# Optimization experiments

Hardware: AMD Instinct MI355X
Metric: run time of the kernel (lower is better)

The kernel has to match this reference:

```python
import jax, jax.numpy as jnp
import numpy as np

N, E = 10000, 320000
IN, HID, HEADS, OUT = 1280, 128, 4, 500
NEG_SLOPE = 0.2
BN_EPS = 1e-5


def gat_layer(x, src, dst, W, a_src, a_dst, b, concat):
    """PyG-style GATConv (single weight matrix, additive attention, scatter-softmax)."""
    n = x.shape[0]
    H, C = a_src.shape
    xp = (x @ W).reshape(n, H, C)                      # [N,H,C]
    s = jnp.sum(xp * a_src, axis=-1)                   # [N,H] src attention logits
    d = jnp.sum(xp * a_dst, axis=-1)                   # [N,H] dst attention logits
    e = jax.nn.leaky_relu(s[src] + d[dst], NEG_SLOPE)  # [Etot,H]
    # scatter-softmax over edges sharing the same destination node
    m = jax.ops.segment_max(e, dst, num_segments=n)
    ex = jnp.exp(e - m[dst])
    z = jax.ops.segment_sum(ex, dst, num_segments=n)
    alpha = ex / z[dst]                                # [Etot,H]
    out = jax.ops.segment_sum(alpha[:, :, None] * xp[src], dst, num_segments=n)  # [N,H,C]
    out = out.reshape(n, H * C) if concat else out.mean(axis=1)
    return out + b


def batch_norm(x, gamma, beta):
    mu = x.mean(axis=0)
    var = x.var(axis=0)  # biased, matches torch BN training normalization
    return (x - mu) * jax.lax.rsqrt(var + BN_EPS) * gamma + beta


def setup_inputs() -> dict:
    key = jax.random.key(0)
    ks = jax.random.split(key, 20)
    rn = lambda k, shape, s=0.05: jax.random.normal(k, shape, jnp.float32) * s
    HC = HID * HEADS
    return {
        "x": jax.random.normal(ks[0], (N, IN), jnp.float32),
        "edge_index": jax.random.randint(ks[1], (2, E), 0, N, jnp.int64 if jax.config.jax_enable_x64 else jnp.int32),
        "W1": rn(ks[2], (IN, HC)), "a_src1": rn(ks[3], (HEADS, HID)), "a_dst1": rn(ks[4], (HEADS, HID)), "b1": jnp.zeros((HC,), jnp.float32),
        "g1": jnp.ones((HC,), jnp.float32), "be1": jnp.zeros((HC,), jnp.float32),
        "W2": rn(ks[5], (HC, HC)), "a_src2": rn(ks[6], (HEADS, HID)), "a_dst2": rn(ks[7], (HEADS, HID)), "b2": jnp.zeros((HC,), jnp.float32),
        "g2": jnp.ones((HC,), jnp.float32), "be2": jnp.zeros((HC,), jnp.float32),
        "W3": rn(ks[8], (HC, OUT)), "a_src3": rn(ks[9], (1, OUT)), "a_dst3": rn(ks[10], (1, OUT)), "b3": jnp.zeros((OUT,), jnp.float32),
    }


def reference(x, edge_index, W1, a_src1, a_dst1, b1, g1, be1,
              W2, a_src2, a_dst2, b2, g2, be2, W3, a_src3, a_dst3, b3):
    n = x.shape[0]
    loops = jnp.arange(n, dtype=edge_index.dtype)
    src = jnp.concatenate([edge_index[0], loops])  # PyG add_self_loops=True
    dst = jnp.concatenate([edge_index[1], loops])
    h = gat_layer(x, src, dst, W1, a_src1, a_dst1, b1, concat=True)
    h = jax.nn.elu(batch_norm(h, g1, be1))
    h = gat_layer(h, src, dst, W2, a_src2, a_dst2, b2, concat=True)
    h = jax.nn.elu(batch_norm(h, g2, be2))
    return gat_layer(h, src, dst, W3, a_src3, a_dst3, b3, concat=False)
```

## Files before the change

kernel.cpp:

```cpp
#include <hip/hip_runtime.h>
#include <hip/hip_bf16.h>

#define NNODES 10000
#define NEDGES 320000
#define INF_   1280
#define HID_   128
#define HEADS_ 4
#define OUTF_  500
#define HC_    512
#define NEG_SLOPE 0.2f
#define BN_EPS 1e-5f

typedef __attribute__((ext_vector_type(8))) short short8x;
typedef __attribute__((ext_vector_type(4))) float f32x4;
typedef unsigned short ushort_t;
typedef unsigned int uint_t;

__device__ __forceinline__ ushort_t f2bf(float f) {
    uint_t u = __float_as_uint(f);
    u = (u + 0x7fffu + ((u >> 16) & 1u)) >> 16;
    return (ushort_t)u;
}
__device__ __forceinline__ float bf_lo(uint_t p) { return __uint_as_float(p << 16); }
__device__ __forceinline__ float bf_hi(uint_t p) { return __uint_as_float(p & 0xffff0000u); }
__device__ __forceinline__ float lrelu(float x) { return (x >= 0.f) ? x : NEG_SLOPE * x; }
__device__ __forceinline__ uint_t pack_bf16_rn(float a, float b) {
    __hip_bfloat162 h = __float22bfloat162_rn(make_float2(a, b));
    return *(uint_t*)&h;
}

__global__ void zero_kernel(float* __restrict__ p, size_t n) {
    size_t i = (size_t)blockIdx.x * blockDim.x + threadIdx.x;
    size_t stride = (size_t)gridDim.x * blockDim.x;
    for (; i < n; i += stride) p[i] = 0.0f;
}

#define CVX (NNODES * INF_ / 4)
#define CN1 (HC_ * INF_)
#define CN2 (HC_ * HC_)
#define CN3 (HC_ * HC_)
__global__ void convall_kernel(const float* __restrict__ x,
                               const float* __restrict__ W1,
                               const float* __restrict__ W2,
                               const float* __restrict__ W3,
                               ushort_t* __restrict__ x_bf,
                               ushort_t* __restrict__ Wt1,
                               ushort_t* __restrict__ Wt2,
                               ushort_t* __restrict__ Wt3) {
    int i = blockIdx.x * blockDim.x + threadIdx.x;
    if (i < CVX) {
        float4 v = ((const float4*)x)[i];
        ((uint2*)x_bf)[i] = make_uint2(pack_bf16_rn(v.x, v.y), pack_bf16_rn(v.z, v.w));
    } else if (i < CVX + CN1) {
        int j = i - CVX;
        int n = j / INF_, k = j - n * INF_;
        Wt1[j] = f2bf(W1[(size_t)k * HC_ + n]);
    } else if (i < CVX + CN1 + CN2) {
        int j = i - CVX - CN1;
        int n = j / HC_, k = j - n * HC_;
        Wt2[j] = f2bf(W2[(size_t)k * HC_ + n]);
    } else if (i < CVX + CN1 + CN2 + CN3) {
        int j = i - CVX - CN1 - CN2;
        int n = j / HC_, k = j - n * HC_;
        Wt3[j] = (n < OUTF_) ? f2bf(W3[(size_t)k * OUTF_ + n]) : (ushort_t)0;
    }
}

__global__ void count_kernel(const int* __restrict__ dst, int* __restrict__ counts, int E) {
    int e = blockIdx.x * blockDim.x + threadIdx.x;
    if (e < E) atomicAdd(&counts[dst[e]], 1);
}

__global__ __launch_bounds__(256) void scan1_kernel(const int* __restrict__ counts,
                                                    int* __restrict__ offsets,
                                                    int* __restrict__ bsum, int n) {
    __shared__ int tmp[256];
    int b = blockIdx.x, t = threadIdx.x;
    int i = b * 256 + t;
    int v = (i < n) ? counts[i] : 0;
    tmp[t] = v;
    __syncthreads();
    for (int off = 1; off < 256; off <<= 1) {
        int u = (t >= off) ? tmp[t - off] : 0;
        __syncthreads();
        tmp[t] += u;
        __syncthreads();
    }
    if (i < n) offsets[i] = tmp[t] - v;
    if (t == 255) bsum[b] = tmp[t];
}

__global__ __launch_bounds__(256) void scan3b_kernel(int* __restrict__ offsets,
                                                     int* __restrict__ cursor,
                                                     const int* __restrict__ bsum,
                                                     int nb, int n) {
    __shared__ int base_sh, tot_sh;
    int b = blockIdx.x, t = threadIdx.x;
    if (t == 0) {
        int acc = 0, tot = 0;
        for (int k = 0; k < nb; ++k) { if (k < b) acc += bsum[k]; tot += bsum[k]; }
        base_sh = acc; tot_sh = tot;
    }
    __syncthreads();
    int i = b * 256 + t;
    if (i < n) {
        int v = offsets[i] + base_sh;
        offsets[i] = v;
        cursor[i] = v;
    }
    if (b == nb - 1 && t == 0) offsets[n] = tot_sh;
}

__global__ void scatter_kernel(const int* __restrict__ src, const int* __restrict__ dst,
                               int* __restrict__ cursor, int* __restrict__ esrc, int E) {
    int e = blockIdx.x * blockDim.x + threadIdx.x;
    if (e < E) {
        int p = atomicAdd(&cursor[dst[e]], 1);
        esrc[p] = src[e];
    }
}

#define LDT 40

__global__ __launch_bounds__(256) void gemm_kernel(
    const ushort_t* __restrict__ A,
    const ushort_t* __restrict__ Bt,
    ushort_t* __restrict__ Cb,
    int M, int K)
{
    __shared__ __align__(16) ushort_t As[64 * LDT];
    __shared__ __align__(16) ushort_t Bs[128 * LDT];

    int m0 = blockIdx.y * 64;
    int n0 = blockIdx.x * 128;

    int tid  = threadIdx.x;
    int lane = tid & 63;
    int w    = tid >> 6;
    int wm   = (w & 1) * 32;
    int wn   = (w >> 1) * 64;
    int quad = lane >> 4;
    int c16  = lane & 15;

    f32x4 acc[2][4];
#pragma unroll
    for (int i = 0; i < 2; ++i)
#pragma unroll
        for (int j = 0; j < 4; ++j)
#pragma unroll
            for (int r = 0; r < 4; ++r) acc[i][j][r] = 0.0f;

    int sr = tid >> 2;
    int sk = (tid & 3) * 8;
    int gm = m0 + sr;  if (gm > M - 1) gm = M - 1;
    const ushort_t* aptr = A + (size_t)gm * K + sk;
    int br0 = tid >> 2;
    int bk0 = (tid & 3) * 8;
    int br1 = (256 + tid) >> 2;
    int bk1 = bk0;
    const ushort_t* bptr0 = Bt + (size_t)(n0 + br0) * K + bk0;
    const ushort_t* bptr1 = Bt + (size_t)(n0 + br1) * K + bk1;

    uint4 av  = *(const uint4*)(aptr);
    uint4 bv0 = *(const uint4*)(bptr0);
    uint4 bv1 = *(const uint4*)(bptr1);

    for (int k0 = 0; k0 < K; k0 += 32) {
        *(uint4*)&As[sr * LDT + sk]   = av;
        *(uint4*)&Bs[br0 * LDT + bk0] = bv0;
        *(uint4*)&Bs[br1 * LDT + bk1] = bv1;
        __syncthreads();

        short8x af0 = *(const short8x*)&As[(wm +      c16) * LDT + quad * 8];
        short8x af1 = *(const short8x*)&As[(wm + 16 + c16) * LDT + quad * 8];
        short8x bf[4];
#pragma unroll
        for (int nt = 0; nt < 4; ++nt)
            bf[nt] = *(const short8x*)&Bs[(wn + nt * 16 + c16) * LDT + quad * 8];

        if (k0 + 32 < K) {
            av  = *(const uint4*)(aptr  + k0 + 32);
            bv0 = *(const uint4*)(bptr0 + k0 + 32);
            bv1 = *(const uint4*)(bptr1 + k0 + 32);
        }

#pragma unroll
        for (int nt = 0; nt < 4; ++nt) {
            acc[0][nt] = __builtin_amdgcn_mfma_f32_16x16x32_bf16(af0, bf[nt], acc[0][nt], 0, 0, 0);
            acc[1][nt] = __builtin_amdgcn_mfma_f32_16x16x32_bf16(af1, bf[nt], acc[1][nt], 0, 0, 0);
        }
        __syncthreads();
    }

#pragma unroll
    for (int mt = 0; mt < 2; ++mt) {
#pragma unroll
        for (int r = 0; r < 4; ++r) {
            int row = m0 + wm + mt * 16 + quad * 4 + r;
            if (row < M) {
#pragma unroll
                for (int nt = 0; nt < 4; ++nt) {
                    int col = n0 + wn + nt * 16 + c16;
                    Cb[(size_t)row * 512 + col] = f2bf(acc[mt][nt][r]);
                }
            }
        }
    }
}

template<int H>
__global__ __launch_bounds__(256) void logits_kernel(
    const uint4* __restrict__ xpb4,
    const float* __restrict__ aS, const float* __restrict__ aD,
    float* __restrict__ s_log, float* __restrict__ d_log, int OUTC)
{
    int node = blockIdx.x * 4 + (threadIdx.x >> 6);
    if (node >= NNODES) return;
    int lane = threadIdx.x & 63;
    uint4 p = xpb4[(size_t)node * 64 + lane];
    float xv[8] = {bf_lo(p.x), bf_hi(p.x), bf_lo(p.y), bf_hi(p.y),
                   bf_lo(p.z), bf_hi(p.z), bf_lo(p.w), bf_hi(p.w)};
    int cbase = lane * 8;
    float sv = 0.f, dv = 0.f;
    if (cbase + 7 < OUTC) {
        float4 a0 = ((const float4*)aS)[lane * 2];
        float4 a1 = ((const float4*)aS)[lane * 2 + 1];
        float4 b0 = ((const float4*)aD)[lane * 2];
        float4 b1 = ((const float4*)aD)[lane * 2 + 1];
        sv = xv[0]*a0.x + xv[1]*a0.y + xv[2]*a0.z + xv[3]*a0.w
           + xv[4]*a1.x + xv[5]*a1.y + xv[6]*a1.z + xv[7]*a1.w;
        dv = xv[0]*b0.x + xv[1]*b0.y + xv[2]*b0.z + xv[3]*b0.w
           + xv[4]*b1.x + xv[5]*b1.y + xv[6]*b1.z + xv[7]*b1.w;
    } else {
#pragma unroll
        for (int k = 0; k < 8; ++k) {
            int c = cbase + k;
            if (c < OUTC) { sv += xv[k] * aS[c]; dv += xv[k] * aD[c]; }
        }
    }
    int grp = (H == 4) ? 16 : 64;
    for (int off = 1; off < grp; off <<= 1) {
        sv += __shfl_xor(sv, off);
        dv += __shfl_xor(dv, off);
    }
    if ((lane & (grp - 1)) == 0) {
        int h = (H == 4) ? (lane >> 4) : 0;
        s_log[node * H + h] = sv;
        d_log[node * H + h] = dv;
    }
}

__device__ __forceinline__ void acc8(float* acc, uint4 q, float w) {
    acc[0] += w * bf_lo(q.x); acc[1] += w * bf_hi(q.x);
    acc[2] += w * bf_lo(q.y); acc[3] += w * bf_hi(q.y);
    acc[4] += w * bf_lo(q.z); acc[5] += w * bf_hi(q.z);
    acc[6] += w * bf_lo(q.w); acc[7] += w * bf_hi(q.w);
}

template<int H>
__global__ __launch_bounds__(256) void gather_fused_kernel(
    const uint4* __restrict__ xpb4,
    const int* __restrict__ offsets, const int* __restrict__ esrc,
    const float* __restrict__ s_log,
    const float* __restrict__ d_log,
    const float* __restrict__ bias,
    float* __restrict__ out,
    int OUTC, int ldo)
{
    int id = blockIdx.x;
    int xcd = id & 7;
    int slice = xcd >> 1;
    int sub2 = xcd & 1;
    int wv = threadIdx.x >> 6;
    int node = (id >> 3) * 8 + sub2 * 4 + wv;
    if (node >= NNODES) return;
    int lane = threadIdx.x & 63;
    int esub = lane >> 4;
    int l16 = lane & 15;
    int h = (H == 4) ? slice : 0;
    int rowoff = slice * 16 + l16;

    float dh = d_log[node * H + h];
    float c0 = lrelu(s_log[node * H + h] + dh);

    float acc[8];
    float z;
    if (esub == 0) {
        uint4 p = xpb4[(size_t)node * 64 + rowoff];
        acc[0] = bf_lo(p.x); acc[1] = bf_hi(p.x);
        acc[2] = bf_lo(p.y); acc[3] = bf_hi(p.y);
        acc[4] = bf_lo(p.z); acc[5] = bf_hi(p.z);
        acc[6] = bf_lo(p.w); acc[7] = bf_hi(p.w);
        z = 1.0f;
    } else {
#pragma unroll
        for (int k = 0; k < 8; ++k) acc[k] = 0.f;
        z = 0.f;
    }

    int e0 = offsets[node], e1 = offsets[node + 1];
    int j = e0 + esub;
    for (; j + 12 < e1; j += 16) {
        int s0 = esrc[j], s1 = esrc[j + 4], s2 = esrc[j + 8], s3 = esrc[j + 12];
        uint4 q0 = xpb4[(size_t)s0 * 64 + rowoff];
        uint4 q1 = xpb4[(size_t)s1 * 64 + rowoff];
        uint4 q2 = xpb4[(size_t)s2 * 64 + rowoff];
        uint4 q3 = xpb4[(size_t)s3 * 64 + rowoff];
        float w0 = __expf(lrelu(s_log[s0 * H + h] + dh) - c0);
        float w1 = __expf(lrelu(s_log[s1 * H + h] + dh) - c0);
        float w2 = __expf(lrelu(s_log[s2 * H + h] + dh) - c0);
        float w3 = __expf(lrelu(s_log[s3 * H + h] + dh) - c0);
        acc8(acc, q0, w0);
        acc8(acc, q1, w1);
        acc8(acc, q2, w2);
        acc8(acc, q3, w3);
        z += w0 + w1 + w2 + w3;
    }
    for (; j < e1; j += 4) {
        int s0 = esrc[j];
        uint4 q0 = xpb4[(size_t)s0 * 64 + rowoff];
        float w0 = __expf(lrelu(s_log[s0 * H + h] + dh) - c0);
        acc8(acc, q0, w0);
        z += w0;
    }

#pragma unroll
    for (int k = 0; k < 8; ++k) {
        acc[k] += __shfl_xor(acc[k], 16);
        acc[k] += __shfl_xor(acc[k], 32);
    }
    z += __shfl_xor(z, 16);
    z += __shfl_xor(z, 32);

    if (esub == 0) {
        float zi = 1.0f / z;
        int cbase = slice * 128 + l16 * 8;
        size_t ob = (size_t)node * ldo + cbase;
        if (cbase + 7 < OUTC) {
            float4 o0 = make_float4(acc[0] * zi + bias[cbase + 0], acc[1] * zi + bias[cbase + 1],
                                    acc[2] * zi + bias[cbase + 2], acc[3] * zi + bias[cbase + 3]);
            float4 o1 = make_float4(acc[4] * zi + bias[cbase + 4], acc[5] * zi + bias[cbase + 5],
                                    acc[6] * zi + bias[cbase + 6], acc[7] * zi + bias[cbase + 7]);
            *(float4*)(out + ob) = o0;
            *(float4*)(out + ob + 4) = o1;
        } else {
#pragma unroll
            for (int k = 0; k < 8; ++k) {
                int c = cbase + k;
                if (c < OUTC) out[ob + k] = acc[k] * zi + bias[c];
            }
        }
    }
}

__global__ __launch_bounds__(512) void bn_stats_kernel(const float* __restrict__ h,
                                                       float* __restrict__ psum,
                                                       float* __restrict__ psumsq) {
    int c = threadIdx.x;
    int b = blockIdx.x;
    float sm = 0.f, sq = 0.f;
    for (int r = b; r < NNODES; r += 64) {
        float v = h[(size_t)r * 512 + c];
        sm += v;
        sq += v * v;
    }
    psum[b * 512 + c] = sm;
    psumsq[b * 512 + c] = sq;
}

__global__ __launch_bounds__(512) void bn_finalize_kernel(const float* __restrict__ psum,
                                                          const float* __restrict__ psumsq,
                                                          const float* __restrict__ gamma,
                                                          const float* __restrict__ beta,
                                                          float* __restrict__ scale,
                                                          float* __restrict__ shift) {
    int c = threadIdx.x;
    float sm = 0.f, sq = 0.f;
    for (int b = 0; b < 64; ++b) {
        sm += psum[b * 512 + c];
        sq += psumsq[b * 512 + c];
    }
    const float invN = 1.0f / (float)NNODES;
    float mu = sm * invN;
    float var = sq * invN - mu * mu;
    float sc = gamma[c] * rsqrtf(var + BN_EPS);
    scale[c] = sc;
    shift[c] = beta[c] - mu * sc;
}

__global__ __launch_bounds__(256) void bn_apply_kernel(const float* __restrict__ h,
                                                       const float* __restrict__ scale,
                                                       const float* __restrict__ shift,
                                                       uint_t* __restrict__ hbf) {
    int t = threadIdx.x, b = blockIdx.x;
    int c0 = t * 2, c1 = c0 + 1;
    float sc0 = scale[c0], sc1 = scale[c1];
    float sh0 = shift[c0], sh1 = shift[c1];
    for (int r = b; r < NNODES; r += 256) {
        float2 hv = ((const float2*)(h + (size_t)r * 512))[t];
        float v0 = hv.x * sc0 + sh0;
        float v1 = hv.y * sc1 + sh1;
        v0 = (v0 > 0.f) ? v0 : (__expf(v0) - 1.0f);
        v1 = (v1 > 0.f) ? v1 : (__expf(v1) - 1.0f);
        hbf[r * 256 + t] = ((uint_t)f2bf(v1) << 16) | (uint_t)f2bf(v0);
    }
}

extern "C" void kernel_launch(void* const* d_in, const int* in_sizes, int n_in,
                              void* d_out, int out_size, void* d_ws, size_t ws_size,
                              hipStream_t stream) {
    const float* x      = (const float*)d_in[0];
    const int*   ei     = (const int*)d_in[1];
    const float* W1     = (const float*)d_in[2];
    const float* a_src1 = (const float*)d_in[3];
    const float* a_dst1 = (const float*)d_in[4];
    const float* b1     = (const float*)d_in[5];
    const float* g1     = (const float*)d_in[6];
    const float* be1    = (const float*)d_in[7];
    const float* W2     = (const float*)d_in[8];
    const float* a_src2 = (const float*)d_in[9];
    const float* a_dst2 = (const float*)d_in[10];
    const float* b2     = (const float*)d_in[11];
    const float* g2     = (const float*)d_in[12];
    const float* be2    = (const float*)d_in[13];
    const float* W3     = (const float*)d_in[14];
    const float* a_src3 = (const float*)d_in[15];
    const float* a_dst3 = (const float*)d_in[16];
    const float* b3     = (const float*)d_in[17];
    float* out = (float*)d_out;

    const int* e_src = ei;
    const int* e_dst = ei + NEDGES;

    char* w = (char*)d_ws;
    ushort_t* x_bf = (ushort_t*)w;
    float*    hbuf = (float*)w;
    w += (size_t)NNODES * INF_ * sizeof(ushort_t);
    uint_t* xpb = (uint_t*)w;  w += (size_t)NNODES * HC_ * sizeof(ushort_t);
    uint_t* hbf = (uint_t*)w;  w += (size_t)NNODES * HC_ * sizeof(ushort_t);
    ushort_t* Wt1 = (ushort_t*)w; w += (size_t)HC_ * INF_ * sizeof(ushort_t);
    ushort_t* Wt2 = (ushort_t*)w; w += (size_t)HC_ * HC_ * sizeof(ushort_t);
    ushort_t* Wt3 = (ushort_t*)w; w += (size_t)HC_ * HC_ * sizeof(ushort_t);
    int* counts  = (int*)w;    w += NNODES * sizeof(int);
    float* s_log = (float*)w;  w += NNODES * HEADS_ * sizeof(float);
    float* d_log = (float*)w;  w += NNODES * HEADS_ * sizeof(float);
    float* bnscale = (float*)w; w += HC_ * sizeof(float);
    float* bnshift = (float*)w; w += HC_ * sizeof(float);
    float* psum  = (float*)w;  w += 64 * HC_ * sizeof(float);
    float* psumsq= (float*)w;  w += 64 * HC_ * sizeof(float);
    int* offsets = (int*)w;    w += (NNODES + 1) * sizeof(int);
    int* cursor  = (int*)w;    w += NNODES * sizeof(int);
    int* esrc    = (int*)w;    w += NEDGES * sizeof(int);
    int* bsum    = (int*)w;    w += 64 * sizeof(int);

    dim3 gg(HC_ / 128, (NNODES + 63) / 64);
    const int lgGrid = (NNODES + 3) / 4;
    const int gaGrid = ((NNODES + 7) / 8) * 8;
    const int scanBlocks = (NNODES + 255) / 256;

    zero_kernel<<<32, 256, 0, stream>>>((float*)counts, NNODES);
    count_kernel<<<(NEDGES + 255) / 256, 256, 0, stream>>>(e_dst, counts, NEDGES);
    scan1_kernel<<<scanBlocks, 256, 0, stream>>>(counts, offsets, bsum, NNODES);
    scan3b_kernel<<<scanBlocks, 256, 0, stream>>>(offsets, cursor, bsum, scanBlocks, NNODES);
    scatter_kernel<<<(NEDGES + 255) / 256, 256, 0, stream>>>(e_src, e_dst, cursor, esrc, NEDGES);
    {
        int TOT = CVX + CN1 + CN2 + CN3;
        convall_kernel<<<(TOT + 255) / 256, 256, 0, stream>>>(x, W1, W2, W3, x_bf, Wt1, Wt2, Wt3);
    }

    gemm_kernel<<<gg, 256, 0, stream>>>(x_bf, Wt1, (ushort_t*)xpb, NNODES, INF_);
    logits_kernel<HEADS_><<<lgGrid, 256, 0, stream>>>((const uint4*)xpb, a_src1, a_dst1, s_log, d_log, HC_);
    gather_fused_kernel<HEADS_><<<gaGrid, 256, 0, stream>>>((const uint4*)xpb, offsets, esrc,
        s_log, d_log, b1, hbuf, HC_, HC_);
    bn_stats_kernel<<<64, 512, 0, stream>>>(hbuf, psum, psumsq);
    bn_finalize_kernel<<<1, 512, 0, stream>>>(psum, psumsq, g1, be1, bnscale, bnshift);
    bn_apply_kernel<<<256, 256, 0, stream>>>(hbuf, bnscale, bnshift, hbf);

    gemm_kernel<<<gg, 256, 0, stream>>>((const ushort_t*)hbf, Wt2, (ushort_t*)xpb, NNODES, HC_);
    logits_kernel<HEADS_><<<lgGrid, 256, 0, stream>>>((const uint4*)xpb, a_src2, a_dst2, s_log, d_log, HC_);
    gather_fused_kernel<HEADS_><<<gaGrid, 256, 0, stream>>>((const uint4*)xpb, offsets, esrc,
        s_log, d_log, b2, hbuf, HC_, HC_);
    bn_stats_kernel<<<64, 512, 0, stream>>>(hbuf, psum, psumsq);
    bn_finalize_kernel<<<1, 512, 0, stream>>>(psum, psumsq, g2, be2, bnscale, bnshift);
    bn_apply_kernel<<<256, 256, 0, stream>>>(hbuf, bnscale, bnshift, hbf);

    gemm_kernel<<<gg, 256, 0, stream>>>((const ushort_t*)hbf, Wt3, (ushort_t*)xpb, NNODES, HC_);
    logits_kernel<1><<<lgGrid, 256, 0, stream>>>((const uint4*)xpb, a_src3, a_dst3, s_log, d_log, OUTF_);
    gather_fused_kernel<1><<<gaGrid, 256, 0, stream>>>((const uint4*)xpb, offsets, esrc,
        s_log, d_log, b3, out, OUTF_, OUTF_);
}
```

Measured before the change: 464.4 us.

## Fuse BN stats into gather, single-block scan, fold zeroing into conversion

BatchNorm statistics are now accumulated with float atomics into 64 banked partial buffers from the gather epilogue, and the finalize step is folded into bn_apply. This removes the separate stats and finalize kernels and one full re-read of the hidden activations. The two-pass scan becomes a single 1024-thread block, and count/partial-buffer zeroing moves into the conversion kernel, cutting several launches. In exchange it adds atomic contention on the partial sums and makes the BN statistics summation order nondeterministic.

```diff
diff --git a/kernel.cpp b/kernel.cpp
--- a/kernel.cpp
+++ b/kernel.cpp
@@ -29,16 +29,12 @@
     return *(uint_t*)&h;
 }
 
-__global__ void zero_kernel(float* __restrict__ p, size_t n) {
-    size_t i = (size_t)blockIdx.x * blockDim.x + threadIdx.x;
-    size_t stride = (size_t)gridDim.x * blockDim.x;
-    for (; i < n; i += stride) p[i] = 0.0f;
-}
-
 #define CVX (NNODES * INF_ / 4)
 #define CN1 (HC_ * INF_)
 #define CN2 (HC_ * HC_)
 #define CN3 (HC_ * HC_)
+#define CZC (NNODES / 4)
+#define CZP (4 * 64 * HC_ / 4)
 __global__ void convall_kernel(const float* __restrict__ x,
                                const float* __restrict__ W1,
                                const float* __restrict__ W2,
@@ -46,7 +42,9 @@
                                ushort_t* __restrict__ x_bf,
                                ushort_t* __restrict__ Wt1,
                                ushort_t* __restrict__ Wt2,
-                               ushort_t* __restrict__ Wt3) {
+                               ushort_t* __restrict__ Wt3,
+                               uint4* __restrict__ zc,
+                               uint4* __restrict__ zp) {
     int i = blockIdx.x * blockDim.x + threadIdx.x;
     if (i < CVX) {
         float4 v = ((const float4*)x)[i];
@@ -63,6 +61,10 @@
         int j = i - CVX - CN1 - CN2;
         int n = j / HC_, k = j - n * HC_;
         Wt3[j] = (n < OUTF_) ? f2bf(W3[(size_t)k * OUTF_ + n]) : (ushort_t)0;
+    } else if (i < CVX + CN1 + CN2 + CN3 + CZC) {
+        zc[i - CVX - CN1 - CN2 - CN3] = make_uint4(0, 0, 0, 0);
+    } else if (i < CVX + CN1 + CN2 + CN3 + CZC + CZP) {
+        zp[i - CVX - CN1 - CN2 - CN3 - CZC] = make_uint4(0, 0, 0, 0);
     }
 }
 
@@ -71,44 +73,40 @@
     if (e < E) atomicAdd(&counts[dst[e]], 1);
 }
 
-__global__ __launch_bounds__(256) void scan1_kernel(const int* __restrict__ counts,
-                                                    int* __restrict__ offsets,
-                                                    int* __restrict__ bsum, int n) {
-    __shared__ int tmp[256];
-    int b = blockIdx.x, t = threadIdx.x;
-    int i = b * 256 + t;
-    int v = (i < n) ? counts[i] : 0;
-    tmp[t] = v;
+__global__ __launch_bounds__(1024) void scan_fused_kernel(const int* __restrict__ counts,
+                                                          int* __restrict__ offsets,
+                                                          int* __restrict__ cursor, int n) {
+    __shared__ int tsum[1024];
+    int t = threadIdx.x;
+    int base = t * 10;
+    int v[10];
+    int s = 0;
+#pragma unroll
+    for (int k = 0; k < 10; ++k) {
+        int i = base + k;
+        int c = (i < n) ? counts[i] : 0;
+        v[k] = s;
+        s += c;
+    }
+    tsum[t] = s;
     __syncthreads();
-    for (int off = 1; off < 256; off <<= 1) {
-        int u = (t >= off) ? tmp[t - off] : 0;
+    for (int off = 1; off < 1024; off <<= 1) {
+        int u = (t >= off) ? tsum[t - off] : 0;
         __syncthreads();
-        tmp[t] += u;
+        tsum[t] += u;
         __syncthreads();
     }
-    if (i < n) offsets[i] = tmp[t] - v;
-    if (t == 255) bsum[b] = tmp[t];
-}
-
-__global__ __launch_bounds__(256) void scan3b_kernel(int* __restrict__ offsets,
-                                                     int* __restrict__ cursor,
-                                                     const int* __restrict__ bsum,
-                                                     int nb, int n) {
-    __shared__ int base_sh, tot_sh;
-    int b = blockIdx.x, t = threadIdx.x;
-    if (t == 0) {
-        int acc = 0, tot = 0;
-        for (int k = 0; k < nb; ++k) { if (k < b) acc += bsum[k]; tot += bsum[k]; }
-        base_sh = acc; tot_sh = tot;
-    }
-    __syncthreads();
-    int i = b * 256 + t;
-    if (i < n) {
-        int v = offsets[i] + base_sh;
-        offsets[i] = v;
-        cursor[i] = v;
-    }
-    if (b == nb - 1 && t == 0) offsets[n] = tot_sh;
+    int prefix = (t > 0) ? tsum[t - 1] : 0;
+#pragma unroll
+    for (int k = 0; k < 10; ++k) {
+        int i = base + k;
+        if (i < n) {
+            int o = prefix + v[k];
+            offsets[i] = o;
+            cursor[i] = o;
+        }
+    }
+    if (t == 1023) offsets[n] = tsum[1023];
 }
 
 __global__ void scatter_kernel(const int* __restrict__ src, const int* __restrict__ dst,
@@ -257,7 +255,7 @@
     acc[6] += w * bf_lo(q.w); acc[7] += w * bf_hi(q.w);
 }
 
-template<int H>
+template<int H, bool BN>
 __global__ __launch_bounds__(256) void gather_fused_kernel(
     const uint4* __restrict__ xpb4,
     const int* __restrict__ offsets, const int* __restrict__ esrc,
@@ -265,6 +263,8 @@
     const float* __restrict__ d_log,
     const float* __restrict__ bias,
     float* __restrict__ out,
+    float* __restrict__ psum,
+    float* __restrict__ psumsq,
     int OUTC, int ldo)
 {
     int id = blockIdx.x;
@@ -336,66 +336,53 @@
         float zi = 1.0f / z;
         int cbase = slice * 128 + l16 * 8;
         size_t ob = (size_t)node * ldo + cbase;
+        float v[8];
+#pragma unroll
+        for (int k = 0; k < 8; ++k) v[k] = acc[k] * zi + bias[cbase + k];
         if (cbase + 7 < OUTC) {
-            float4 o0 = make_float4(acc[0] * zi + bias[cbase + 0], acc[1] * zi + bias[cbase + 1],
-                                    acc[2] * zi + bias[cbase + 2], acc[3] * zi + bias[cbase + 3]);
-            float4 o1 = make_float4(acc[4] * zi + bias[cbase + 4], acc[5] * zi + bias[cbase + 5],
-                                    acc[6] * zi + bias[cbase + 6], acc[7] * zi + bias[cbase + 7]);
-            *(float4*)(out + ob) = o0;
-            *(float4*)(out + ob + 4) = o1;
+            *(float4*)(out + ob)     = make_float4(v[0], v[1], v[2], v[3]);
+            *(float4*)(out + ob + 4) = make_float4(v[4], v[5], v[6], v[7]);
         } else {
 #pragma unroll
             for (int k = 0; k < 8; ++k) {
                 int c = cbase + k;
-                if (c < OUTC) out[ob + k] = acc[k] * zi + bias[c];
+                if (c < OUTC) out[ob + k] = v[k];
             }
         }
-    }
-}
-
-__global__ __launch_bounds__(512) void bn_stats_kernel(const float* __restrict__ h,
-                                                       float* __restrict__ psum,
-                                                       float* __restrict__ psumsq) {
-    int c = threadIdx.x;
-    int b = blockIdx.x;
-    float sm = 0.f, sq = 0.f;
-    for (int r = b; r < NNODES; r += 64) {
-        float v = h[(size_t)r * 512 + c];
-        sm += v;
-        sq += v * v;
-    }
-    psum[b * 512 + c] = sm;
-    psumsq[b * 512 + c] = sq;
-}
-
-__global__ __launch_bounds__(512) void bn_finalize_kernel(const float* __restrict__ psum,
-                                                          const float* __restrict__ psumsq,
-                                                          const float* __restrict__ gamma,
-                                                          const float* __restrict__ beta,
-                                                          float* __restrict__ scale,
-                                                          float* __restrict__ shift) {
-    int c = threadIdx.x;
-    float sm = 0.f, sq = 0.f;
-    for (int b = 0; b < 64; ++b) {
-        sm += psum[b * 512 + c];
-        sq += psumsq[b * 512 + c];
-    }
-    const float invN = 1.0f / (float)NNODES;
-    float mu = sm * invN;
-    float var = sq * invN - mu * mu;
-    float sc = gamma[c] * rsqrtf(var + BN_EPS);
-    scale[c] = sc;
-    shift[c] = beta[c] - mu * sc;
+        if (BN) {
+            int bank = (id >> 3) & 63;
+            float* ps  = psum   + (size_t)bank * 512 + cbase;
+            float* psq = psumsq + (size_t)bank * 512 + cbase;
+#pragma unroll
+            for (int k = 0; k < 8; ++k) {
+                atomicAdd(&ps[k], v[k]);
+                atomicAdd(&psq[k], v[k] * v[k]);
+            }
+        }
+    }
 }
 
 __global__ __launch_bounds__(256) void bn_apply_kernel(const float* __restrict__ h,
-                                                       const float* __restrict__ scale,
-                                                       const float* __restrict__ shift,
+                                                       const float* __restrict__ psum,
+                                                       const float* __restrict__ psumsq,
+                                                       const float* __restrict__ gamma,
+                                                       const float* __restrict__ beta,
                                                        uint_t* __restrict__ hbf) {
     int t = threadIdx.x, b = blockIdx.x;
     int c0 = t * 2, c1 = c0 + 1;
-    float sc0 = scale[c0], sc1 = scale[c1];
-    float sh0 = shift[c0], sh1 = shift[c1];
+    float sm0 = 0.f, sq0 = 0.f, sm1 = 0.f, sq1 = 0.f;
+    for (int k = 0; k < 64; ++k) {
+        sm0 += psum[k * 512 + c0];   sq0 += psumsq[k * 512 + c0];
+        sm1 += psum[k * 512 + c1];   sq1 += psumsq[k * 512 + c1];
+    }
+    const float invN = 1.0f / (float)NNODES;
+    float mu0 = sm0 * invN, mu1 = sm1 * invN;
+    float var0 = sq0 * invN - mu0 * mu0;
+    float var1 = sq1 * invN - mu1 * mu1;
+    float sc0 = gamma[c0] * rsqrtf(var0 + BN_EPS);
+    float sc1 = gamma[c1] * rsqrtf(var1 + BN_EPS);
+    float sh0 = beta[c0] - mu0 * sc0;
+    float sh1 = beta[c1] - mu1 * sc1;
     for (int r = b; r < NNODES; r += 256) {
         float2 hv = ((const float2*)(h + (size_t)r * 512))[t];
         float v0 = hv.x * sc0 + sh0;
@@ -444,48 +431,43 @@
     int* counts  = (int*)w;    w += NNODES * sizeof(int);
     float* s_log = (float*)w;  w += NNODES * HEADS_ * sizeof(float);
     float* d_log = (float*)w;  w += NNODES * HEADS_ * sizeof(float);
-    float* bnscale = (float*)w; w += HC_ * sizeof(float);
-    float* bnshift = (float*)w; w += HC_ * sizeof(float);
-    float* psum  = (float*)w;  w += 64 * HC_ * sizeof(float);
-    float* psumsq= (float*)w;  w += 64 * HC_ * sizeof(float);
+    float* psumall = (float*)w; w += (size_t)4 * 64 * HC_ * sizeof(float);
     int* offsets = (int*)w;    w += (NNODES + 1) * sizeof(int);
     int* cursor  = (int*)w;    w += NNODES * sizeof(int);
     int* esrc    = (int*)w;    w += NEDGES * sizeof(int);
-    int* bsum    = (int*)w;    w += 64 * sizeof(int);
+
+    float* psum1   = psumall;
+    float* psumsq1 = psumall + 64 * HC_;
+    float* psum2   = psumall + 2 * 64 * HC_;
+    float* psumsq2 = psumall + 3 * 64 * HC_;
 
     dim3 gg(HC_ / 128, (NNODES + 63) / 64);
     const int lgGrid = (NNODES + 3) / 4;
     const int gaGrid = ((NNODES + 7) / 8) * 8;
-    const int scanBlocks = (NNODES + 255) / 256;
-
-    zero_kernel<<<32, 256, 0, stream>>>((float*)counts, NNODES);
+
+    {
+        int TOT = CVX + CN1 + CN2 + CN3 + CZC + CZP;
+        convall_kernel<<<(TOT + 255) / 256, 256, 0, stream>>>(x, W1, W2, W3,
+            x_bf, Wt1, Wt2, Wt3, (uint4*)counts, (uint4*)psumall);
+    }
     count_kernel<<<(NEDGES + 255) / 256, 256, 0, stream>>>(e_dst, counts, NEDGES);
-    scan1_kernel<<<scanBlocks, 256, 0, stream>>>(counts, offsets, bsum, NNODES);
-    scan3b_kernel<<<scanBlocks, 256, 0, stream>>>(offsets, cursor, bsum, scanBlocks, NNODES);
+    scan_fused_kernel<<<1, 1024, 0, stream>>>(counts, offsets, cursor, NNODES);
     scatter_kernel<<<(NEDGES + 255) / 256, 256, 0, stream>>>(e_src, e_dst, cursor, esrc, NEDGES);
-    {
-        int TOT = CVX + CN1 + CN2 + CN3;
-        convall_kernel<<<(TOT + 255) / 256, 256, 0, stream>>>(x, W1, W2, W3, x_bf, Wt1, Wt2, Wt3);
-    }
 
     gemm_kernel<<<gg, 256, 0, stream>>>(x_bf, Wt1, (ushort_t*)xpb, NNODES, INF_);
     logits_kernel<HEADS_><<<lgGrid, 256, 0, stream>>>((const uint4*)xpb, a_src1, a_dst1, s_log, d_log, HC_);
-    gather_fused_kernel<HEADS_><<<gaGrid, 256, 0, stream>>>((const uint4*)xpb, offsets, esrc,
-        s_log, d_log, b1, hbuf, HC_, HC_);
-    bn_stats_kernel<<<64, 512, 0, stream>>>(hbuf, psum, psumsq);
-    bn_finalize_kernel<<<1, 512, 0, stream>>>(psum, psumsq, g1, be1, bnscale, bnshift);
-    bn_apply_kernel<<<256, 256, 0, stream>>>(hbuf, bnscale, bnshift, hbf);
+    gather_fused_kernel<HEADS_, true><<<gaGrid, 256, 0, stream>>>((const uint4*)xpb, offsets, esrc,
+        s_log, d_log, b1, hbuf, psum1, psumsq1, HC_, HC_);
+    bn_apply_kernel<<<256, 256, 0, stream>>>(hbuf, psum1, psumsq1, g1, be1, hbf);
 
     gemm_kernel<<<gg, 256, 0, stream>>>((const ushort_t*)hbf, Wt2, (ushort_t*)xpb, NNODES, HC_);
     logits_kernel<HEADS_><<<lgGrid, 256, 0, stream>>>((const uint4*)xpb, a_src2, a_dst2, s_log, d_log, HC_);
-    gather_fused_kernel<HEADS_><<<gaGrid, 256, 0, stream>>>((const uint4*)xpb, offsets, esrc,
-        s_log, d_log, b2, hbuf, HC_, HC_);
-    bn_stats_kernel<<<64, 512, 0, stream>>>(hbuf, psum, psumsq);
-    bn_finalize_kernel<<<1, 512, 0, stream>>>(psum, psumsq, g2, be2, bnscale, bnshift);
-    bn_apply_kernel<<<256, 256, 0, stream>>>(hbuf, bnscale, bnshift, hbf);
+    gather_fused_kernel<HEADS_, true><<<gaGrid, 256, 0, stream>>>((const uint4*)xpb, offsets, esrc,
+        s_log, d_log, b2, hbuf, psum2, psumsq2, HC_, HC_);
+    bn_apply_kernel<<<256, 256, 0, stream>>>(hbuf, psum2, psumsq2, g2, be2, hbf);
 
     gemm_kernel<<<gg, 256, 0, stream>>>((const ushort_t*)hbf, Wt3, (ushort_t*)xpb, NNODES, HC_);
     logits_kernel<1><<<lgGrid, 256, 0, stream>>>((const uint4*)xpb, a_src3, a_dst3, s_log, d_log, OUTF_);
-    gather_fused_kernel<1><<<gaGrid, 256, 0, stream>>>((const uint4*)xpb, offsets, esrc,
-        s_log, d_log, b3, out, OUTF_, OUTF_);
-}
+    gather_fused_kernel<1, false><<<gaGrid, 256, 0, stream>>>((const uint4*)xpb, offsets, esrc,
+        s_log, d_log, b3, out, nullptr, nullptr, OUTF_, OUTF_);
+}
```

New measurement: 908.9 us. +95.7%, slower.
